# Kernel tuning notes

Measured on AMD Instinct MI355X. Metric: run time of the kernel, lower is better.

## Reference

```python
import jax, jax.numpy as jnp
import numpy as np

N, E, C, H = 50000, 800000, 64, 64
EPS = 1e-5


def _edge_conv(x, src, dst, Wa, ba, Wb, bb):
    # PyG EdgeConv: h_i = max_{j in N(i)} MLP([x_i, x_j - x_i]), aggr='max'
    xi = x[dst]                      # [E, C] target features
    xj = x[src]                      # [E, C] source features
    h = jnp.concatenate([xi, xj - xi], axis=-1)   # [E, 2C]
    h = jax.nn.relu(h @ Wa + ba)
    h = jax.nn.relu(h @ Wb + bb)     # [E, H]
    out = jax.ops.segment_max(h, dst, num_segments=x.shape[0])
    # nodes with no incoming edge: segment_max yields -inf -> fill with 0
    return jnp.where(jnp.isneginf(out), 0.0, out)


def _batchnorm(x, gamma, beta):
    # training-mode BatchNorm1d: biased batch stats over the node dim
    mean = jnp.mean(x, axis=0)
    var = jnp.var(x, axis=0)
    return gamma * (x - mean) * jax.lax.rsqrt(var + EPS) + beta


def setup_inputs() -> dict:
    key = jax.random.key(0)
    ks = jax.random.split(key, 12)
    x = jax.random.normal(ks[0], (N, C), dtype=jnp.float32)
    edge_index = jax.random.randint(ks[1], (2, E), 0, N, dtype=jnp.int64)
    batch = jnp.zeros((N,), dtype=jnp.int64)
    s1 = 1.0 / np.sqrt(2 * C)
    s2 = 1.0 / np.sqrt(H)
    return {
        "x": x,
        "edge_index": edge_index,
        "batch": batch,
        "W1a": jax.random.normal(ks[2], (2 * C, H), jnp.float32) * s1,
        "b1a": jnp.zeros((H,), jnp.float32),
        "W1b": jax.random.normal(ks[3], (H, H), jnp.float32) * s2,
        "b1b": jnp.zeros((H,), jnp.float32),
        "gamma1": jnp.ones((H,), jnp.float32),
        "beta1": jnp.zeros((H,), jnp.float32),
        "W2a": jax.random.normal(ks[4], (2 * H, H), jnp.float32) * s2,
        "b2a": jnp.zeros((H,), jnp.float32),
        "W2b": jax.random.normal(ks[5], (H, H), jnp.float32) * s2,
        "b2b": jnp.zeros((H,), jnp.float32),
        "gamma2": jnp.ones((H,), jnp.float32),
        "beta2": jnp.zeros((H,), jnp.float32),
    }


def reference(x, edge_index, batch, W1a, b1a, W1b, b1b, gamma1, beta1,
              W2a, b2a, W2b, b2b, gamma2, beta2):
    src, dst = edge_index[0], edge_index[1]
    h = _edge_conv(x, src, dst, W1a, b1a, W1b, b1b)
    h = _batchnorm(h, gamma1, beta1)
    h = _edge_conv(h, src, dst, W2a, b2a, W2b, b2b)
    h = _batchnorm(h, gamma2, beta2)
    return h
```

## Files before the change

### kernel.cpp

```cpp
#include <hip/hip_runtime.h>
#include <hip/hip_bf16.h>

typedef float f32x4 __attribute__((ext_vector_type(4)));
typedef short s16x8 __attribute__((ext_vector_type(8)));

#define EPS 1e-5f

__device__ __forceinline__ unsigned short f32_to_bf16_rne(float f) {
    unsigned u = __float_as_uint(f);
    unsigned r = u + 0x7FFFu + ((u >> 16) & 1u);
    return (unsigned short)(r >> 16);
}

__device__ __forceinline__ unsigned cvtpk(float a, float b) {
    unsigned d;
    asm("v_cvt_pk_bf16_f32 %0, %1, %2" : "=v"(d) : "v"(a), "v"(b));
    return d;
}

#define DPPF(v, c) __int_as_float(__builtin_amdgcn_update_dpp(0, __float_as_int(v), (c), 0xF, 0xF, true))
#define SWZ4(v) __int_as_float(__builtin_amdgcn_ds_swizzle(__float_as_int(v), 0x101F))

__global__ void pack_all(const float* __restrict__ W1a, const float* __restrict__ W1b,
                         const float* __restrict__ W2a, const float* __restrict__ W2b,
                         unsigned short* __restrict__ p, float* __restrict__ stats,
                         int* __restrict__ count, int N) {
    int idx = blockIdx.x * 256 + threadIdx.x;
    if (idx < 24576) {
        int m = idx >> 12;
        int t = idx & 4095;
        int j = t & 7;
        int lane = (t >> 3) & 63;
        int mt = (t >> 9) & 3;
        int kc = t >> 11;
        int k = kc * 32 + (lane >> 4) * 8 + j;
        int c = mt * 16 + (lane & 15);
        float v;
        switch (m) {
            case 0: v = W1a[k * 64 + c] - W1a[(k + 64) * 64 + c]; break;
            case 1: v = W1a[(k + 64) * 64 + c]; break;
            case 2: v = W1b[k * 64 + c]; break;
            case 3: v = W2a[k * 64 + c] - W2a[(k + 64) * 64 + c]; break;
            case 4: v = W2a[(k + 64) * 64 + c]; break;
            default: v = W2b[k * 64 + c]; break;
        }
        p[idx] = f32_to_bf16_rne(v);
    } else if (idx < 24832) {
        stats[idx - 24576] = 0.f;
    } else if (idx - 24832 < N) {
        count[idx - 24832] = 0;
    }
}

__global__ void cvt_hist(const float* __restrict__ in, unsigned short* __restrict__ out, int n4,
                         const int* __restrict__ edst, int* __restrict__ count, int E) {
    int i = blockIdx.x * 256 + threadIdx.x;
    if (i < n4) {
        f32x4 v = ((const f32x4*)in)[i];
        uint2 pr;
        pr.x = cvtpk(v[0], v[1]);
        pr.y = cvtpk(v[2], v[3]);
        *(uint2*)(out + i * 4) = pr;
    }
    if (i < E) atomicAdd(&count[edst[i]], 1);
}

__global__ void scan1(const int* __restrict__ count, int* __restrict__ offsets,
                      int* __restrict__ bsums, int N) {
    __shared__ int sdata[256];
    int t = threadIdx.x;
    int base = blockIdx.x * 1024 + t * 4;
    int4 v = {0, 0, 0, 0};
    if (base + 3 < N) {
        v = *(const int4*)(count + base);
    } else {
        if (base + 0 < N) v.x = count[base + 0];
        if (base + 1 < N) v.y = count[base + 1];
        if (base + 2 < N) v.z = count[base + 2];
    }
    int s = v.x + v.y + v.z + v.w;
    sdata[t] = s;
    __syncthreads();
    for (int off = 1; off < 256; off <<= 1) {
        int u = (t >= off) ? sdata[t - off] : 0;
        __syncthreads();
        sdata[t] += u;
        __syncthreads();
    }
    int excl = sdata[t] - s;
    if (t == 255) bsums[blockIdx.x] = sdata[255];
    int o0 = excl;
    int o1 = o0 + v.x;
    int o2 = o1 + v.y;
    int o3 = o2 + v.z;
    if (base + 0 < N) offsets[base + 0] = o0;
    if (base + 1 < N) offsets[base + 1] = o1;
    if (base + 2 < N) offsets[base + 2] = o2;
    if (base + 3 < N) offsets[base + 3] = o3;
}

__global__ void scan2(int* __restrict__ bsums, int* __restrict__ offsets, int N, int nb) {
    __shared__ int sdata[256];
    int t = threadIdx.x;
    int s = (t < nb) ? bsums[t] : 0;
    sdata[t] = s;
    __syncthreads();
    for (int off = 1; off < 256; off <<= 1) {
        int u = (t >= off) ? sdata[t - off] : 0;
        __syncthreads();
        sdata[t] += u;
        __syncthreads();
    }
    if (t < nb) bsums[t] = sdata[t] - s;
    if (t == 255) offsets[N] = sdata[255];
}

__global__ void scan3(int* __restrict__ offsets, int* __restrict__ cursor,
                      const int* __restrict__ bsums, int N) {
    int i = blockIdx.x * 256 + threadIdx.x;
    if (i < N) {
        int v = offsets[i] + bsums[i >> 10];
        offsets[i] = v;
        cursor[i] = v;
    }
}

__global__ void scatter_kernel(const int* __restrict__ esrc, const int* __restrict__ edst,
                               int* __restrict__ cursor, int* __restrict__ ssrc, int E) {
    int i = blockIdx.x * 256 + threadIdx.x;
    if (i < E) {
        int d = edst[i];
        int pos = atomicAdd(&cursor[d], 1);
        ssrc[pos] = esrc[i];
    }
}

#define LSTR 88
__global__ __launch_bounds__(256, 3) void edgeconv_sorted(
    const unsigned short* __restrict__ xb,
    const int* __restrict__ ssrc,
    const int* __restrict__ offsets,
    const unsigned short* __restrict__ pWxi,
    const unsigned short* __restrict__ pWxj,
    const unsigned short* __restrict__ pWb,
    const float* __restrict__ ba,
    const float* __restrict__ bb,
    float* __restrict__ out,
    float* __restrict__ statsOut,
    int N) {
    __shared__ __align__(16) unsigned short xh[4][16 * LSTR];
    __shared__ float sred[128];
    const int tid = threadIdx.x;
    const int w = tid >> 6;
    const int lane = tid & 63;
    const int g = lane >> 4;
    const int r = lane & 15;
    const int srow = lane >> 2;
    const int schk = lane & 3;

    if (tid < 128) sred[tid] = 0.f;
    __syncthreads();

    s16x8 axj[2][4], ab[2][4];
#pragma unroll
    for (int kc = 0; kc < 2; ++kc)
#pragma unroll
        for (int mt = 0; mt < 4; ++mt) {
            axj[kc][mt] = *(const s16x8*)(pWxj + ((kc * 4 + mt) * 64 + lane) * 8);
            ab[kc][mt] = *(const s16x8*)(pWb + ((kc * 4 + mt) * 64 + lane) * 8);
        }

    unsigned short* myb = xh[w];
    const int totalWaves = gridDim.x * 4;
    const f32x4 zf = {0.f, 0.f, 0.f, 0.f};

    const int ch = (r >> 2) * 16 + g * 4 + (r & 3);
    const float b2l = bb[ch];
    float bsum = 0.f, bss = 0.f;

    for (int node = blockIdx.x * 4 + w; node < N; node += totalWaves) {
        const int segB = offsets[node];
        const int segE = offsets[node + 1];

        f32x4 rm[4];
#pragma unroll
        for (int mt = 0; mt < 4; ++mt)
            rm[mt] = (f32x4){-INFINITY, -INFINITY, -INFINITY, -INFINITY};

        if (segB < segE) {
            int sv = ssrc[min(segB + srow, segE - 1)];
            s16x8 ra = *(const s16x8*)(xb + sv * 64 + schk * 8);
            s16x8 rb = *(const s16x8*)(xb + sv * 64 + 32 + schk * 8);

            s16x8 xi1 = *(const s16x8*)(xb + node * 64 + g * 8);
            s16x8 xi2 = *(const s16x8*)(xb + node * 64 + 32 + g * 8);
            f32x4 accxi[4];
#pragma unroll
            for (int mt = 0; mt < 4; ++mt)
                accxi[mt] = *(const f32x4*)(ba + mt * 16 + g * 4);
#pragma unroll
            for (int mt = 0; mt < 4; ++mt) {
                s16x8 f0 = *(const s16x8*)(pWxi + ((0 * 4 + mt) * 64 + lane) * 8);
                accxi[mt] = __builtin_amdgcn_mfma_f32_16x16x32_bf16(f0, xi1, accxi[mt], 0, 0, 0);
                s16x8 f1 = *(const s16x8*)(pWxi + ((1 * 4 + mt) * 64 + lane) * 8);
                accxi[mt] = __builtin_amdgcn_mfma_f32_16x16x32_bf16(f1, xi2, accxi[mt], 0, 0, 0);
            }

            for (int t0 = segB; t0 < segE; t0 += 16) {
                *(s16x8*)(myb + srow * LSTR + schk * 8) = ra;
                *(s16x8*)(myb + srow * LSTR + 32 + schk * 8) = rb;
                s16x8 xj1 = *(const s16x8*)(myb + r * LSTR + g * 8);
                s16x8 xj2 = *(const s16x8*)(myb + r * LSTR + 32 + g * 8);

                int t1 = t0 + 16;
                if (t1 < segE) {
                    int sv2 = ssrc[min(t1 + srow, segE - 1)];
                    ra = *(const s16x8*)(xb + sv2 * 64 + schk * 8);
                    rb = *(const s16x8*)(xb + sv2 * 64 + 32 + schk * 8);
                }

                f32x4 acc[4];
#pragma unroll
                for (int mt = 0; mt < 4; ++mt) {
                    acc[mt] = __builtin_amdgcn_mfma_f32_16x16x32_bf16(axj[0][mt], xj1, accxi[mt], 0, 0, 0);
                    acc[mt] = __builtin_amdgcn_mfma_f32_16x16x32_bf16(axj[1][mt], xj2, acc[mt], 0, 0, 0);
                }

#pragma unroll
                for (int mt = 0; mt < 4; ++mt) {
                    uint2 pr;
                    pr.x = cvtpk(fmaxf(acc[mt][0], 0.f), fmaxf(acc[mt][1], 0.f));
                    pr.y = cvtpk(fmaxf(acc[mt][2], 0.f), fmaxf(acc[mt][3], 0.f));
                    *(uint2*)(myb + r * LSTR + mt * 16 + g * 4) = pr;
                }
                s16x8 p0 = *(const s16x8*)(myb + r * LSTR + g * 8);
                s16x8 p1 = *(const s16x8*)(myb + r * LSTR + 32 + g * 8);

                f32x4 acc2[4];
#pragma unroll
                for (int mt = 0; mt < 4; ++mt) {
                    acc2[mt] = __builtin_amdgcn_mfma_f32_16x16x32_bf16(ab[0][mt], p0, zf, 0, 0, 0);
                    acc2[mt] = __builtin_amdgcn_mfma_f32_16x16x32_bf16(ab[1][mt], p1, acc2[mt], 0, 0, 0);
                }

#pragma unroll
                for (int mt = 0; mt < 4; ++mt)
#pragma unroll
                    for (int q = 0; q < 4; ++q)
                        rm[mt][q] = fmaxf(rm[mt][q], acc2[mt][q]);
            }
        }

        float k8[8];
#pragma unroll
        for (int j = 0; j < 8; ++j) {
            float lo = rm[j >> 2][j & 3];
            float hv = rm[(j >> 2) + 2][j & 3];
            float tlo = DPPF(lo, 0x128);
            float thi = DPPF(hv, 0x128);
            float own = (r & 8) ? hv : lo;
            float oth = (r & 8) ? thi : tlo;
            k8[j] = fmaxf(own, oth);
        }
        float k4[4];
#pragma unroll
        for (int j = 0; j < 4; ++j) {
            float ta = SWZ4(k8[j]);
            float tb = SWZ4(k8[j + 4]);
            float own = (r & 4) ? k8[j + 4] : k8[j];
            float oth = (r & 4) ? tb : ta;
            k4[j] = fmaxf(own, oth);
        }
        float k2[2];
#pragma unroll
        for (int j = 0; j < 2; ++j) {
            float ta = DPPF(k4[j], 0x4E);
            float tb = DPPF(k4[j + 2], 0x4E);
            float own = (r & 2) ? k4[j + 2] : k4[j];
            float oth = (r & 2) ? tb : ta;
            k2[j] = fmaxf(own, oth);
        }
        float ta = DPPF(k2[0], 0xB1);
        float tb = DPPF(k2[1], 0xB1);
        float vfin = fmaxf((r & 1) ? k2[1] : k2[0], (r & 1) ? tb : ta);

        float o = fmaxf(vfin + b2l, 0.f);
        out[node * 64 + ch] = o;
        bsum += o;
        bss += o * o;
    }

    atomicAdd(&sred[ch], bsum);
    atomicAdd(&sred[64 + ch], bss);
    __syncthreads();
    if (tid < 128) atomicAdd(&statsOut[tid], sred[tid]);
}

__global__ void bn_apply(const float* __restrict__ in, const float* __restrict__ stats,
                         const float* __restrict__ gamma, const float* __restrict__ beta,
                         unsigned short* __restrict__ outb, float* __restrict__ outf,
                         int n4, float invN) {
    int i = blockIdx.x * 256 + threadIdx.x;
    if (i >= n4) return;
    int c0 = (i * 4) & 63;
    f32x4 v = ((const f32x4*)in)[i];
    f32x4 o;
#pragma unroll
    for (int q = 0; q < 4; ++q) {
        int c = c0 + q;
        float mean = stats[c] * invN;
        float var = stats[64 + c] * invN - mean * mean;
        float sc = gamma[c] * rsqrtf(var + EPS);
        o[q] = (v[q] - mean) * sc + beta[c];
    }
    if (outb) {
        uint2 pr;
        pr.x = cvtpk(o[0], o[1]);
        pr.y = cvtpk(o[2], o[3]);
        *(uint2*)(outb + i * 4) = pr;
    } else {
        ((f32x4*)outf)[i] = o;
    }
}

extern "C" void kernel_launch(void* const* d_in, const int* in_sizes, int n_in,
                              void* d_out, int out_size, void* d_ws, size_t ws_size,
                              hipStream_t stream) {
    const float* x = (const float*)d_in[0];
    const int* ei = (const int*)d_in[1];
    const float* W1a = (const float*)d_in[3];
    const float* b1a = (const float*)d_in[4];
    const float* W1b = (const float*)d_in[5];
    const float* b1b = (const float*)d_in[6];
    const float* gamma1 = (const float*)d_in[7];
    const float* beta1 = (const float*)d_in[8];
    const float* W2a = (const float*)d_in[9];
    const float* b2a = (const float*)d_in[10];
    const float* W2b = (const float*)d_in[11];
    const float* b2b = (const float*)d_in[12];
    const float* gamma2 = (const float*)d_in[13];
    const float* beta2 = (const float*)d_in[14];

    const int N = in_sizes[0] / 64;
    const int E = in_sizes[1] / 2;
    const int NC = N * 64;

    char* ws = (char*)d_ws;
    size_t off = 0;
    auto alloc = [&](size_t bytes) {
        char* p = ws + off;
        off += (bytes + 255) & ~(size_t)255;
        return p;
    };
    float* acc = (float*)alloc((size_t)NC * 4);
    unsigned short* xb = (unsigned short*)alloc((size_t)NC * 2);
    unsigned short* pw = (unsigned short*)alloc(24576 * 2);
    float* stats = (float*)alloc(256 * 4);
    int* count = (int*)alloc((size_t)N * 4);
    int* offsets = (int*)alloc((size_t)(N + 1) * 4);
    int* cursor = (int*)alloc((size_t)(N + 1) * 4);
    int* ssrc = (int*)alloc((size_t)E * 4);
    int* bsums = (int*)alloc(1024 * 4);

    const int* esrc = ei;
    const int* edst = ei + E;

    int pgrid = (24832 + N + 255) / 256;
    pack_all<<<pgrid, 256, 0, stream>>>(W1a, W1b, W2a, W2b, pw, stats, count, N);

    int n4 = NC / 4;
    int big = max(n4, E);
    cvt_hist<<<(big + 255) / 256, 256, 0, stream>>>(x, xb, n4, edst, count, E);

    int nb = (N + 1023) / 1024;
    scan1<<<nb, 256, 0, stream>>>(count, offsets, bsums, N);
    scan2<<<1, 256, 0, stream>>>(bsums, offsets, N, nb);
    scan3<<<(N + 255) / 256, 256, 0, stream>>>(offsets, cursor, bsums, N);
    scatter_kernel<<<(E + 255) / 256, 256, 0, stream>>>(esrc, edst, cursor, ssrc, E);

    int cgrid = (n4 + 255) / 256;
    const int egrid = 2048;

    edgeconv_sorted<<<egrid, 256, 0, stream>>>(xb, ssrc, offsets, pw, pw + 4096, pw + 8192,
                                               b1a, b1b, acc, stats, N);
    bn_apply<<<cgrid, 256, 0, stream>>>(acc, stats, gamma1, beta1, xb, nullptr, n4, 1.0f / N);

    edgeconv_sorted<<<egrid, 256, 0, stream>>>(xb, ssrc, offsets, pw + 12288, pw + 16384,
                                               pw + 20480, b2a, b2b, (float*)d_out, stats + 128, N);
    bn_apply<<<cgrid, 256, 0, stream>>>((float*)d_out, stats + 128, gamma2, beta2, nullptr,
                                        (float*)d_out, n4, 1.0f / N);
}
```

Baseline: 267.6 us.

## Process two destination nodes per wave iteration to interleave independent MFMA chains

Each wave now handles a contiguous block of nodes, two at a time. The two nodes' gathers, MFMA chains, LDS staging and max-reductions are interleaved in one loop whose trip count is the larger of the two tile counts. The aim is to hide MFMA dependency latency and gather latency by giving the scheduler two independent streams of work. In exchange, the shorter segment does redundant work up to the longer one's tile count, register pressure roughly doubles, LDS per wave doubles, and the grid shrinks to 1792 blocks with a contiguous node partition.

```diff
diff --git a/kernel.cpp b/kernel.cpp
--- a/kernel.cpp
+++ b/kernel.cpp
@@ -147,8 +147,8 @@
     const float* __restrict__ bb,
     float* __restrict__ out,
     float* __restrict__ statsOut,
-    int N) {
-    __shared__ __align__(16) unsigned short xh[4][16 * LSTR];
+    int N, int npw) {
+    __shared__ __align__(16) unsigned short xh[4][2 * 16 * LSTR];
     __shared__ float sred[128];
     const int tid = threadIdx.x;
     const int w = tid >> 6;
@@ -170,124 +170,184 @@
             ab[kc][mt] = *(const s16x8*)(pWb + ((kc * 4 + mt) * 64 + lane) * 8);
         }
 
-    unsigned short* myb = xh[w];
-    const int totalWaves = gridDim.x * 4;
+    unsigned short* mybA = xh[w];
+    unsigned short* mybB = xh[w] + 16 * LSTR;
     const f32x4 zf = {0.f, 0.f, 0.f, 0.f};
 
     const int ch = (r >> 2) * 16 + g * 4 + (r & 3);
     const float b2l = bb[ch];
     float bsum = 0.f, bss = 0.f;
 
-    for (int node = blockIdx.x * 4 + w; node < N; node += totalWaves) {
-        const int segB = offsets[node];
-        const int segE = offsets[node + 1];
-
-        f32x4 rm[4];
+    const int wid = blockIdx.x * 4 + w;
+    const int nodeBase = wid * npw;
+    const int pairs = npw >> 1;
+
+    for (int p = 0; p < pairs; ++p) {
+        const int nA = nodeBase + 2 * p;
+        if (nA >= N) break;
+        const int nB = nA + 1;
+        const bool hasB = nB < N;
+
+        const int sBA = offsets[nA];
+        const int sEA = offsets[nA + 1];
+        const int sBB = hasB ? sEA : sBA;
+        const int sEB = hasB ? offsets[nB + 1] : sEA;
+        const bool vA = sEA > sBA;
+        const bool vB = hasB && (sEB > sBB);
+        const int ntA = max(1, (sEA - sBA + 15) >> 4);
+        const int ntB = max(1, (sEB - sBB + 15) >> 4);
+        const int nt = max(ntA, ntB);
+
+        int ivA = max(min(sBA + srow, sEA - 1), 0);
+        int ivB = max(min(sBB + srow, sEB - 1), 0);
+        int svA = ssrc[ivA];
+        int svB = ssrc[ivB];
+        s16x8 raA = *(const s16x8*)(xb + svA * 64 + schk * 8);
+        s16x8 rbA = *(const s16x8*)(xb + svA * 64 + 32 + schk * 8);
+        s16x8 raB = *(const s16x8*)(xb + svB * 64 + schk * 8);
+        s16x8 rbB = *(const s16x8*)(xb + svB * 64 + 32 + schk * 8);
+
+        const int rowB = min(nB, N - 1);
+        s16x8 xiA1 = *(const s16x8*)(xb + nA * 64 + g * 8);
+        s16x8 xiA2 = *(const s16x8*)(xb + nA * 64 + 32 + g * 8);
+        s16x8 xiB1 = *(const s16x8*)(xb + rowB * 64 + g * 8);
+        s16x8 xiB2 = *(const s16x8*)(xb + rowB * 64 + 32 + g * 8);
+        f32x4 accxiA[4], accxiB[4];
+#pragma unroll
+        for (int mt = 0; mt < 4; ++mt) {
+            f32x4 bias = *(const f32x4*)(ba + mt * 16 + g * 4);
+            s16x8 f0 = *(const s16x8*)(pWxi + ((0 * 4 + mt) * 64 + lane) * 8);
+            s16x8 f1 = *(const s16x8*)(pWxi + ((1 * 4 + mt) * 64 + lane) * 8);
+            f32x4 cA = __builtin_amdgcn_mfma_f32_16x16x32_bf16(f0, xiA1, bias, 0, 0, 0);
+            accxiA[mt] = __builtin_amdgcn_mfma_f32_16x16x32_bf16(f1, xiA2, cA, 0, 0, 0);
+            f32x4 cB = __builtin_amdgcn_mfma_f32_16x16x32_bf16(f0, xiB1, bias, 0, 0, 0);
+            accxiB[mt] = __builtin_amdgcn_mfma_f32_16x16x32_bf16(f1, xiB2, cB, 0, 0, 0);
+        }
+
+        f32x4 rmA[4], rmB[4];
+#pragma unroll
+        for (int mt = 0; mt < 4; ++mt) {
+            rmA[mt] = (f32x4){-INFINITY, -INFINITY, -INFINITY, -INFINITY};
+            rmB[mt] = (f32x4){-INFINITY, -INFINITY, -INFINITY, -INFINITY};
+        }
+
+        for (int it = 0; it < nt; ++it) {
+            *(s16x8*)(mybA + srow * LSTR + schk * 8) = raA;
+            *(s16x8*)(mybA + srow * LSTR + 32 + schk * 8) = rbA;
+            *(s16x8*)(mybB + srow * LSTR + schk * 8) = raB;
+            *(s16x8*)(mybB + srow * LSTR + 32 + schk * 8) = rbB;
+            s16x8 xjA1 = *(const s16x8*)(mybA + r * LSTR + g * 8);
+            s16x8 xjA2 = *(const s16x8*)(mybA + r * LSTR + 32 + g * 8);
+            s16x8 xjB1 = *(const s16x8*)(mybB + r * LSTR + g * 8);
+            s16x8 xjB2 = *(const s16x8*)(mybB + r * LSTR + 32 + g * 8);
+
+            if (it + 1 < nt) {
+                int tA2 = sBA + 16 * min(it + 1, ntA - 1);
+                int tB2 = sBB + 16 * min(it + 1, ntB - 1);
+                int iA2 = max(min(tA2 + srow, sEA - 1), 0);
+                int iB2 = max(min(tB2 + srow, sEB - 1), 0);
+                int sA2 = ssrc[iA2];
+                int sB2 = ssrc[iB2];
+                raA = *(const s16x8*)(xb + sA2 * 64 + schk * 8);
+                rbA = *(const s16x8*)(xb + sA2 * 64 + 32 + schk * 8);
+                raB = *(const s16x8*)(xb + sB2 * 64 + schk * 8);
+                rbB = *(const s16x8*)(xb + sB2 * 64 + 32 + schk * 8);
+            }
+
+            f32x4 accA[4], accB[4];
+#pragma unroll
+            for (int mt = 0; mt < 4; ++mt) {
+                accA[mt] = __builtin_amdgcn_mfma_f32_16x16x32_bf16(axj[0][mt], xjA1, accxiA[mt], 0, 0, 0);
+                accA[mt] = __builtin_amdgcn_mfma_f32_16x16x32_bf16(axj[1][mt], xjA2, accA[mt], 0, 0, 0);
+                accB[mt] = __builtin_amdgcn_mfma_f32_16x16x32_bf16(axj[0][mt], xjB1, accxiB[mt], 0, 0, 0);
+                accB[mt] = __builtin_amdgcn_mfma_f32_16x16x32_bf16(axj[1][mt], xjB2, accB[mt], 0, 0, 0);
+            }
+
+#pragma unroll
+            for (int mt = 0; mt < 4; ++mt) {
+                uint2 prA, prB;
+                prA.x = cvtpk(fmaxf(accA[mt][0], 0.f), fmaxf(accA[mt][1], 0.f));
+                prA.y = cvtpk(fmaxf(accA[mt][2], 0.f), fmaxf(accA[mt][3], 0.f));
+                *(uint2*)(mybA + r * LSTR + mt * 16 + g * 4) = prA;
+                prB.x = cvtpk(fmaxf(accB[mt][0], 0.f), fmaxf(accB[mt][1], 0.f));
+                prB.y = cvtpk(fmaxf(accB[mt][2], 0.f), fmaxf(accB[mt][3], 0.f));
+                *(uint2*)(mybB + r * LSTR + mt * 16 + g * 4) = prB;
+            }
+            s16x8 pA0 = *(const s16x8*)(mybA + r * LSTR + g * 8);
+            s16x8 pA1 = *(const s16x8*)(mybA + r * LSTR + 32 + g * 8);
+            s16x8 pB0 = *(const s16x8*)(mybB + r * LSTR + g * 8);
+            s16x8 pB1 = *(const s16x8*)(mybB + r * LSTR + 32 + g * 8);
+
+            f32x4 acc2A[4], acc2B[4];
+#pragma unroll
+            for (int mt = 0; mt < 4; ++mt) {
+                acc2A[mt] = __builtin_amdgcn_mfma_f32_16x16x32_bf16(ab[0][mt], pA0, zf, 0, 0, 0);
+                acc2A[mt] = __builtin_amdgcn_mfma_f32_16x16x32_bf16(ab[1][mt], pA1, acc2A[mt], 0, 0, 0);
+                acc2B[mt] = __builtin_amdgcn_mfma_f32_16x16x32_bf16(ab[0][mt], pB0, zf, 0, 0, 0);
+                acc2B[mt] = __builtin_amdgcn_mfma_f32_16x16x32_bf16(ab[1][mt], pB1, acc2B[mt], 0, 0, 0);
+            }
+
+#pragma unroll
+            for (int mt = 0; mt < 4; ++mt)
+#pragma unroll
+                for (int q = 0; q < 4; ++q) {
+                    rmA[mt][q] = fmaxf(rmA[mt][q], acc2A[mt][q]);
+                    rmB[mt][q] = fmaxf(rmB[mt][q], acc2B[mt][q]);
+                }
+        }
+
 #pragma unroll
         for (int mt = 0; mt < 4; ++mt)
-            rm[mt] = (f32x4){-INFINITY, -INFINITY, -INFINITY, -INFINITY};
-
-        if (segB < segE) {
-            int sv = ssrc[min(segB + srow, segE - 1)];
-            s16x8 ra = *(const s16x8*)(xb + sv * 64 + schk * 8);
-            s16x8 rb = *(const s16x8*)(xb + sv * 64 + 32 + schk * 8);
-
-            s16x8 xi1 = *(const s16x8*)(xb + node * 64 + g * 8);
-            s16x8 xi2 = *(const s16x8*)(xb + node * 64 + 32 + g * 8);
-            f32x4 accxi[4];
-#pragma unroll
-            for (int mt = 0; mt < 4; ++mt)
-                accxi[mt] = *(const f32x4*)(ba + mt * 16 + g * 4);
-#pragma unroll
-            for (int mt = 0; mt < 4; ++mt) {
-                s16x8 f0 = *(const s16x8*)(pWxi + ((0 * 4 + mt) * 64 + lane) * 8);
-                accxi[mt] = __builtin_amdgcn_mfma_f32_16x16x32_bf16(f0, xi1, accxi[mt], 0, 0, 0);
-                s16x8 f1 = *(const s16x8*)(pWxi + ((1 * 4 + mt) * 64 + lane) * 8);
-                accxi[mt] = __builtin_amdgcn_mfma_f32_16x16x32_bf16(f1, xi2, accxi[mt], 0, 0, 0);
-            }
-
-            for (int t0 = segB; t0 < segE; t0 += 16) {
-                *(s16x8*)(myb + srow * LSTR + schk * 8) = ra;
-                *(s16x8*)(myb + srow * LSTR + 32 + schk * 8) = rb;
-                s16x8 xj1 = *(const s16x8*)(myb + r * LSTR + g * 8);
-                s16x8 xj2 = *(const s16x8*)(myb + r * LSTR + 32 + g * 8);
-
-                int t1 = t0 + 16;
-                if (t1 < segE) {
-                    int sv2 = ssrc[min(t1 + srow, segE - 1)];
-                    ra = *(const s16x8*)(xb + sv2 * 64 + schk * 8);
-                    rb = *(const s16x8*)(xb + sv2 * 64 + 32 + schk * 8);
-                }
-
-                f32x4 acc[4];
-#pragma unroll
-                for (int mt = 0; mt < 4; ++mt) {
-                    acc[mt] = __builtin_amdgcn_mfma_f32_16x16x32_bf16(axj[0][mt], xj1, accxi[mt], 0, 0, 0);
-                    acc[mt] = __builtin_amdgcn_mfma_f32_16x16x32_bf16(axj[1][mt], xj2, acc[mt], 0, 0, 0);
-                }
-
-#pragma unroll
-                for (int mt = 0; mt < 4; ++mt) {
-                    uint2 pr;
-                    pr.x = cvtpk(fmaxf(acc[mt][0], 0.f), fmaxf(acc[mt][1], 0.f));
-                    pr.y = cvtpk(fmaxf(acc[mt][2], 0.f), fmaxf(acc[mt][3], 0.f));
-                    *(uint2*)(myb + r * LSTR + mt * 16 + g * 4) = pr;
-                }
-                s16x8 p0 = *(const s16x8*)(myb + r * LSTR + g * 8);
-                s16x8 p1 = *(const s16x8*)(myb + r * LSTR + 32 + g * 8);
-
-                f32x4 acc2[4];
-#pragma unroll
-                for (int mt = 0; mt < 4; ++mt) {
-                    acc2[mt] = __builtin_amdgcn_mfma_f32_16x16x32_bf16(ab[0][mt], p0, zf, 0, 0, 0);
-                    acc2[mt] = __builtin_amdgcn_mfma_f32_16x16x32_bf16(ab[1][mt], p1, acc2[mt], 0, 0, 0);
-                }
-
-#pragma unroll
-                for (int mt = 0; mt < 4; ++mt)
-#pragma unroll
-                    for (int q = 0; q < 4; ++q)
-                        rm[mt][q] = fmaxf(rm[mt][q], acc2[mt][q]);
-            }
-        }
-
-        float k8[8];
-#pragma unroll
-        for (int j = 0; j < 8; ++j) {
-            float lo = rm[j >> 2][j & 3];
-            float hv = rm[(j >> 2) + 2][j & 3];
-            float tlo = DPPF(lo, 0x128);
-            float thi = DPPF(hv, 0x128);
-            float own = (r & 8) ? hv : lo;
-            float oth = (r & 8) ? thi : tlo;
-            k8[j] = fmaxf(own, oth);
-        }
-        float k4[4];
-#pragma unroll
-        for (int j = 0; j < 4; ++j) {
-            float ta = SWZ4(k8[j]);
-            float tb = SWZ4(k8[j + 4]);
-            float own = (r & 4) ? k8[j + 4] : k8[j];
-            float oth = (r & 4) ? tb : ta;
-            k4[j] = fmaxf(own, oth);
-        }
-        float k2[2];
-#pragma unroll
-        for (int j = 0; j < 2; ++j) {
-            float ta = DPPF(k4[j], 0x4E);
-            float tb = DPPF(k4[j + 2], 0x4E);
-            float own = (r & 2) ? k4[j + 2] : k4[j];
-            float oth = (r & 2) ? tb : ta;
-            k2[j] = fmaxf(own, oth);
-        }
-        float ta = DPPF(k2[0], 0xB1);
-        float tb = DPPF(k2[1], 0xB1);
-        float vfin = fmaxf((r & 1) ? k2[1] : k2[0], (r & 1) ? tb : ta);
-
-        float o = fmaxf(vfin + b2l, 0.f);
-        out[node * 64 + ch] = o;
-        bsum += o;
-        bss += o * o;
+#pragma unroll
+            for (int q = 0; q < 4; ++q) {
+                rmA[mt][q] = vA ? rmA[mt][q] : -INFINITY;
+                rmB[mt][q] = vB ? rmB[mt][q] : -INFINITY;
+            }
+
+#pragma unroll
+        for (int nsel = 0; nsel < 2; ++nsel) {
+            const f32x4* rm = nsel ? rmB : rmA;
+            float k8[8];
+#pragma unroll
+            for (int j = 0; j < 8; ++j) {
+                float lo = rm[j >> 2][j & 3];
+                float hv = rm[(j >> 2) + 2][j & 3];
+                float tlo = DPPF(lo, 0x128);
+                float thi = DPPF(hv, 0x128);
+                float own = (r & 8) ? hv : lo;
+                float oth = (r & 8) ? thi : tlo;
+                k8[j] = fmaxf(own, oth);
+            }
+            float k4[4];
+#pragma unroll
+            for (int j = 0; j < 4; ++j) {
+                float ta = SWZ4(k8[j]);
+                float tb = SWZ4(k8[j + 4]);
+                float own = (r & 4) ? k8[j + 4] : k8[j];
+                float oth = (r & 4) ? tb : ta;
+                k4[j] = fmaxf(own, oth);
+            }
+            float k2[2];
+#pragma unroll
+            for (int j = 0; j < 2; ++j) {
+                float ta = DPPF(k4[j], 0x4E);
+                float tb = DPPF(k4[j + 2], 0x4E);
+                float own = (r & 2) ? k4[j + 2] : k4[j];
+                float oth = (r & 2) ? tb : ta;
+                k2[j] = fmaxf(own, oth);
+            }
+            float ta = DPPF(k2[0], 0xB1);
+            float tb = DPPF(k2[1], 0xB1);
+            float vfin = fmaxf((r & 1) ? k2[1] : k2[0], (r & 1) ? tb : ta);
+
+            float o = fmaxf(vfin + b2l, 0.f);
+            int node = nsel ? nB : nA;
+            if (!nsel || hasB) {
+                out[node * 64 + ch] = o;
+                bsum += o;
+                bss += o * o;
+            }
+        }
     }
 
     atomicAdd(&sred[ch], bsum);
@@ -379,14 +439,18 @@
     scatter_kernel<<<(E + 255) / 256, 256, 0, stream>>>(esrc, edst, cursor, ssrc, E);
 
     int cgrid = (n4 + 255) / 256;
-    const int egrid = 2048;
+    const int egrid = 1792;
+    const int tw = egrid * 4;
+    int npw = (N + tw - 1) / tw;
+    npw = ((npw + 1) / 2) * 2;
 
     edgeconv_sorted<<<egrid, 256, 0, stream>>>(xb, ssrc, offsets, pw, pw + 4096, pw + 8192,
-                                               b1a, b1b, acc, stats, N);
+                                               b1a, b1b, acc, stats, N, npw);
     bn_apply<<<cgrid, 256, 0, stream>>>(acc, stats, gamma1, beta1, xb, nullptr, n4, 1.0f / N);
 
     edgeconv_sorted<<<egrid, 256, 0, stream>>>(xb, ssrc, offsets, pw + 12288, pw + 16384,
-                                               pw + 20480, b2a, b2b, (float*)d_out, stats + 128, N);
+                                               pw + 20480, b2a, b2b, (float*)d_out, stats + 128,
+                                               N, npw);
     bn_apply<<<cgrid, 256, 0, stream>>>((float*)d_out, stats + 128, gamma2, beta2, nullptr,
                                         (float*)d_out, n4, 1.0f / N);
 }
```

Result: slower. 405.3 us (+51.4%).

## Prefetch next node's segment and features; keep Wxi and bias in registers

Applied to the files above, without the earlier changes.

The edgeconv loop now loads the next node's offsets, first source-row features and own features while the current node is being processed, hiding gather latency across loop iterations. The Wxi weight fragments and first-layer bias are hoisted into registers once instead of being reloaded per node. The extra live registers force launch bounds to drop from 3 to 2 waves-per-SIMD minimum, which lowers occupancy in exchange for software pipelining.

```diff
diff --git a/kernel.cpp b/kernel.cpp
--- a/kernel.cpp
+++ b/kernel.cpp
@@ -136,7 +136,7 @@
 }
 
 #define LSTR 88
-__global__ __launch_bounds__(256, 3) void edgeconv_sorted(
+__global__ __launch_bounds__(256, 2) void edgeconv_sorted(
     const unsigned short* __restrict__ xb,
     const int* __restrict__ ssrc,
     const int* __restrict__ offsets,
@@ -161,14 +161,18 @@
     if (tid < 128) sred[tid] = 0.f;
     __syncthreads();
 
-    s16x8 axj[2][4], ab[2][4];
+    s16x8 awxi[2][4], axj[2][4], ab[2][4];
 #pragma unroll
     for (int kc = 0; kc < 2; ++kc)
 #pragma unroll
         for (int mt = 0; mt < 4; ++mt) {
+            awxi[kc][mt] = *(const s16x8*)(pWxi + ((kc * 4 + mt) * 64 + lane) * 8);
             axj[kc][mt] = *(const s16x8*)(pWxj + ((kc * 4 + mt) * 64 + lane) * 8);
             ab[kc][mt] = *(const s16x8*)(pWb + ((kc * 4 + mt) * 64 + lane) * 8);
         }
+    f32x4 bias1r[4];
+#pragma unroll
+    for (int mt = 0; mt < 4; ++mt) bias1r[mt] = *(const f32x4*)(ba + mt * 16 + g * 4);
 
     unsigned short* myb = xh[w];
     const int totalWaves = gridDim.x * 4;
@@ -178,9 +182,34 @@
     const float b2l = bb[ch];
     float bsum = 0.f, bss = 0.f;
 
-    for (int node = blockIdx.x * 4 + w; node < N; node += totalWaves) {
-        const int segB = offsets[node];
-        const int segE = offsets[node + 1];
+    const int node0 = blockIdx.x * 4 + w;
+    int segB = 0, segE = 0;
+    s16x8 ra = {}, rb = {}, xi1 = {}, xi2 = {};
+    if (node0 < N) {
+        segB = offsets[node0];
+        segE = offsets[node0 + 1];
+        int iv = max(min(segB + srow, segE - 1), 0);
+        int sv = ssrc[iv];
+        ra = *(const s16x8*)(xb + sv * 64 + schk * 8);
+        rb = *(const s16x8*)(xb + sv * 64 + 32 + schk * 8);
+        xi1 = *(const s16x8*)(xb + node0 * 64 + g * 8);
+        xi2 = *(const s16x8*)(xb + node0 * 64 + 32 + g * 8);
+    }
+
+    for (int node = node0; node < N; node += totalWaves) {
+        const int nodeN = node + totalWaves;
+        int segBn = 0, segEn = 0;
+        s16x8 ran = {}, rbn = {}, xin1 = {}, xin2 = {};
+        if (nodeN < N) {
+            segBn = offsets[nodeN];
+            segEn = offsets[nodeN + 1];
+            int ivn = max(min(segBn + srow, segEn - 1), 0);
+            int svn = ssrc[ivn];
+            ran = *(const s16x8*)(xb + svn * 64 + schk * 8);
+            rbn = *(const s16x8*)(xb + svn * 64 + 32 + schk * 8);
+            xin1 = *(const s16x8*)(xb + nodeN * 64 + g * 8);
+            xin2 = *(const s16x8*)(xb + nodeN * 64 + 32 + g * 8);
+        }
 
         f32x4 rm[4];
 #pragma unroll
@@ -188,22 +217,11 @@
             rm[mt] = (f32x4){-INFINITY, -INFINITY, -INFINITY, -INFINITY};
 
         if (segB < segE) {
-            int sv = ssrc[min(segB + srow, segE - 1)];
-            s16x8 ra = *(const s16x8*)(xb + sv * 64 + schk * 8);
-            s16x8 rb = *(const s16x8*)(xb + sv * 64 + 32 + schk * 8);
-
-            s16x8 xi1 = *(const s16x8*)(xb + node * 64 + g * 8);
-            s16x8 xi2 = *(const s16x8*)(xb + node * 64 + 32 + g * 8);
             f32x4 accxi[4];
 #pragma unroll
-            for (int mt = 0; mt < 4; ++mt)
-                accxi[mt] = *(const f32x4*)(ba + mt * 16 + g * 4);
-#pragma unroll
             for (int mt = 0; mt < 4; ++mt) {
-                s16x8 f0 = *(const s16x8*)(pWxi + ((0 * 4 + mt) * 64 + lane) * 8);
-                accxi[mt] = __builtin_amdgcn_mfma_f32_16x16x32_bf16(f0, xi1, accxi[mt], 0, 0, 0);
-                s16x8 f1 = *(const s16x8*)(pWxi + ((1 * 4 + mt) * 64 + lane) * 8);
-                accxi[mt] = __builtin_amdgcn_mfma_f32_16x16x32_bf16(f1, xi2, accxi[mt], 0, 0, 0);
+                f32x4 c = __builtin_amdgcn_mfma_f32_16x16x32_bf16(awxi[0][mt], xi1, bias1r[mt], 0, 0, 0);
+                accxi[mt] = __builtin_amdgcn_mfma_f32_16x16x32_bf16(awxi[1][mt], xi2, c, 0, 0, 0);
             }
 
             for (int t0 = segB; t0 < segE; t0 += 16) {
@@ -288,6 +306,13 @@
         out[node * 64 + ch] = o;
         bsum += o;
         bss += o * o;
+
+        segB = segBn;
+        segE = segEn;
+        ra = ran;
+        rb = rbn;
+        xi1 = xin1;
+        xi2 = xin2;
     }
 
     atomicAdd(&sred[ch], bsum);
```

New measurement: 275.4 us. 1.03x slower.

## Fold first BatchNorm into second EdgeConv weights and bias

Applied to the files above, without the earlier changes.

Drops the first bn_apply pass. The first EdgeConv now writes its raw ReLU output straight to bf16, and a small single-block kernel scales the second layer's W2a rows by the BN scale and folds the BN shift into an adjusted bias. This holds because BN is affine per channel and feeds linearly into the first matmul, and the shift cancels in the x_j - x_i half. It removes one full read-fp32/write-bf16 pass over the node features and one launch. The cost is a serial one-block repack kernel and bf16 rounding applied before normalization rather than after, which could change accuracy somewhat.

```diff
diff --git a/kernel.cpp b/kernel.cpp
--- a/kernel.cpp
+++ b/kernel.cpp
@@ -21,12 +21,11 @@
 #define DPPF(v, c) __int_as_float(__builtin_amdgcn_update_dpp(0, __float_as_int(v), (c), 0xF, 0xF, true))
 #define SWZ4(v) __int_as_float(__builtin_amdgcn_ds_swizzle(__float_as_int(v), 0x101F))
 
-__global__ void pack_all(const float* __restrict__ W1a, const float* __restrict__ W1b,
-                         const float* __restrict__ W2a, const float* __restrict__ W2b,
-                         unsigned short* __restrict__ p, float* __restrict__ stats,
-                         int* __restrict__ count, int N) {
+__global__ void pack_zero(const float* __restrict__ W1a, const float* __restrict__ W1b,
+                          const float* __restrict__ W2b, unsigned short* __restrict__ p,
+                          float* __restrict__ stats, int* __restrict__ count, int N) {
     int idx = blockIdx.x * 256 + threadIdx.x;
-    if (idx < 24576) {
+    if (idx < 16384) {
         int m = idx >> 12;
         int t = idx & 4095;
         int j = t & 7;
@@ -36,19 +35,18 @@
         int k = kc * 32 + (lane >> 4) * 8 + j;
         int c = mt * 16 + (lane & 15);
         float v;
+        int dst;
         switch (m) {
-            case 0: v = W1a[k * 64 + c] - W1a[(k + 64) * 64 + c]; break;
-            case 1: v = W1a[(k + 64) * 64 + c]; break;
-            case 2: v = W1b[k * 64 + c]; break;
-            case 3: v = W2a[k * 64 + c] - W2a[(k + 64) * 64 + c]; break;
-            case 4: v = W2a[(k + 64) * 64 + c]; break;
-            default: v = W2b[k * 64 + c]; break;
-        }
-        p[idx] = f32_to_bf16_rne(v);
-    } else if (idx < 24832) {
-        stats[idx - 24576] = 0.f;
-    } else if (idx - 24832 < N) {
-        count[idx - 24832] = 0;
+            case 0: v = W1a[k * 64 + c] - W1a[(k + 64) * 64 + c]; dst = t; break;
+            case 1: v = W1a[(k + 64) * 64 + c]; dst = 4096 + t; break;
+            case 2: v = W1b[k * 64 + c]; dst = 8192 + t; break;
+            default: v = W2b[k * 64 + c]; dst = 20480 + t; break;
+        }
+        p[dst] = f32_to_bf16_rne(v);
+    } else if (idx < 16640) {
+        stats[idx - 16384] = 0.f;
+    } else if (idx - 16640 < N) {
+        count[idx - 16640] = 0;
     }
 }
 
@@ -135,6 +133,51 @@
     }
 }
 
+__global__ void repack2(const float* __restrict__ stats, const float* __restrict__ gamma1,
+                        const float* __restrict__ beta1, const float* __restrict__ W2a,
+                        const float* __restrict__ b2a, unsigned short* __restrict__ pw2,
+                        float* __restrict__ b2adj, float invN) {
+    __shared__ float sc[64], sh[64];
+    __shared__ float part[4][64];
+    int tid = threadIdx.x;
+    if (tid < 64) {
+        float mean = stats[tid] * invN;
+        float var = stats[64 + tid] * invN - mean * mean;
+        float s = gamma1[tid] * rsqrtf(var + EPS);
+        sc[tid] = s;
+        sh[tid] = beta1[tid] - mean * s;
+    }
+    __syncthreads();
+    {
+        int c = tid & 63, sl = tid >> 6;
+        float a = 0.f;
+#pragma unroll
+        for (int kk = 0; kk < 16; ++kk) {
+            int k = sl * 16 + kk;
+            a += sh[k] * W2a[k * 64 + c];
+        }
+        part[sl][c] = a;
+    }
+    __syncthreads();
+    if (tid < 64)
+        b2adj[tid] = b2a[tid] + part[0][tid] + part[1][tid] + part[2][tid] + part[3][tid];
+
+    for (int e = tid; e < 8192; e += 256) {
+        int m = e >> 12;
+        int t = e & 4095;
+        int j = t & 7;
+        int lane = (t >> 3) & 63;
+        int mt = (t >> 9) & 3;
+        int kc = t >> 11;
+        int k = kc * 32 + (lane >> 4) * 8 + j;
+        int c = mt * 16 + (lane & 15);
+        float wtop = W2a[k * 64 + c];
+        float wbot = W2a[(k + 64) * 64 + c];
+        float v = (m == 0) ? sc[k] * (wtop - wbot) : sc[k] * wbot;
+        pw2[e] = f32_to_bf16_rne(v);
+    }
+}
+
 #define LSTR 88
 __global__ __launch_bounds__(256, 3) void edgeconv_sorted(
     const unsigned short* __restrict__ xb,
@@ -145,7 +188,8 @@
     const unsigned short* __restrict__ pWb,
     const float* __restrict__ ba,
     const float* __restrict__ bb,
-    float* __restrict__ out,
+    float* __restrict__ outf,
+    unsigned short* __restrict__ outb,
     float* __restrict__ statsOut,
     int N) {
     __shared__ __align__(16) unsigned short xh[4][16 * LSTR];
@@ -285,7 +329,10 @@
         float vfin = fmaxf((r & 1) ? k2[1] : k2[0], (r & 1) ? tb : ta);
 
         float o = fmaxf(vfin + b2l, 0.f);
-        out[node * 64 + ch] = o;
+        if (outb)
+            outb[node * 64 + ch] = f32_to_bf16_rne(o);
+        else
+            outf[node * 64 + ch] = o;
         bsum += o;
         bss += o * o;
     }
@@ -298,8 +345,7 @@
 
 __global__ void bn_apply(const float* __restrict__ in, const float* __restrict__ stats,
                          const float* __restrict__ gamma, const float* __restrict__ beta,
-                         unsigned short* __restrict__ outb, float* __restrict__ outf,
-                         int n4, float invN) {
+                         float* __restrict__ outf, int n4, float invN) {
     int i = blockIdx.x * 256 + threadIdx.x;
     if (i >= n4) return;
     int c0 = (i * 4) & 63;
@@ -313,14 +359,7 @@
         float sc = gamma[c] * rsqrtf(var + EPS);
         o[q] = (v[q] - mean) * sc + beta[c];
     }
-    if (outb) {
-        uint2 pr;
-        pr.x = cvtpk(o[0], o[1]);
-        pr.y = cvtpk(o[2], o[3]);
-        *(uint2*)(outb + i * 4) = pr;
-    } else {
-        ((f32x4*)outf)[i] = o;
-    }
+    ((f32x4*)outf)[i] = o;
 }
 
 extern "C" void kernel_launch(void* const* d_in, const int* in_sizes, int n_in,
@@ -352,10 +391,11 @@
         off += (bytes + 255) & ~(size_t)255;
         return p;
     };
-    float* acc = (float*)alloc((size_t)NC * 4);
-    unsigned short* xb = (unsigned short*)alloc((size_t)NC * 2);
+    unsigned short* xb1 = (unsigned short*)alloc((size_t)NC * 2);
+    unsigned short* xb2 = (unsigned short*)alloc((size_t)NC * 2);
     unsigned short* pw = (unsigned short*)alloc(24576 * 2);
     float* stats = (float*)alloc(256 * 4);
+    float* b2adj = (float*)alloc(64 * 4);
     int* count = (int*)alloc((size_t)N * 4);
     int* offsets = (int*)alloc((size_t)(N + 1) * 4);
     int* cursor = (int*)alloc((size_t)(N + 1) * 4);
@@ -365,12 +405,12 @@
     const int* esrc = ei;
     const int* edst = ei + E;
 
-    int pgrid = (24832 + N + 255) / 256;
-    pack_all<<<pgrid, 256, 0, stream>>>(W1a, W1b, W2a, W2b, pw, stats, count, N);
+    int pgrid = (16640 + N + 255) / 256;
+    pack_zero<<<pgrid, 256, 0, stream>>>(W1a, W1b, W2b, pw, stats, count, N);
 
     int n4 = NC / 4;
     int big = max(n4, E);
-    cvt_hist<<<(big + 255) / 256, 256, 0, stream>>>(x, xb, n4, edst, count, E);
+    cvt_hist<<<(big + 255) / 256, 256, 0, stream>>>(x, xb1, n4, edst, count, E);
 
     int nb = (N + 1023) / 1024;
     scan1<<<nb, 256, 0, stream>>>(count, offsets, bsums, N);
@@ -378,15 +418,18 @@
     scan3<<<(N + 255) / 256, 256, 0, stream>>>(offsets, cursor, bsums, N);
     scatter_kernel<<<(E + 255) / 256, 256, 0, stream>>>(esrc, edst, cursor, ssrc, E);
 
+    const int egrid = 2048;
+
+    edgeconv_sorted<<<egrid, 256, 0, stream>>>(xb1, ssrc, offsets, pw, pw + 4096, pw + 8192,
+                                               b1a, b1b, nullptr, xb2, stats, N);
+
+    repack2<<<1, 256, 0, stream>>>(stats, gamma1, beta1, W2a, b2a, pw + 12288, b2adj, 1.0f / N);
+
+    edgeconv_sorted<<<egrid, 256, 0, stream>>>(xb2, ssrc, offsets, pw + 12288, pw + 16384,
+                                               pw + 20480, b2adj, b2b, (float*)d_out, nullptr,
+                                               stats + 128, N);
+
     int cgrid = (n4 + 255) / 256;
-    const int egrid = 2048;
-
-    edgeconv_sorted<<<egrid, 256, 0, stream>>>(xb, ssrc, offsets, pw, pw + 4096, pw + 8192,
-                                               b1a, b1b, acc, stats, N);
-    bn_apply<<<cgrid, 256, 0, stream>>>(acc, stats, gamma1, beta1, xb, nullptr, n4, 1.0f / N);
-
-    edgeconv_sorted<<<egrid, 256, 0, stream>>>(xb, ssrc, offsets, pw + 12288, pw + 16384,
-                                               pw + 20480, b2a, b2b, (float*)d_out, stats + 128, N);
-    bn_apply<<<cgrid, 256, 0, stream>>>((float*)d_out, stats + 128, gamma2, beta2, nullptr,
+    bn_apply<<<cgrid, 256, 0, stream>>>((float*)d_out, stats + 128, gamma2, beta2,
                                         (float*)d_out, n4, 1.0f / N);
 }
```

New measurement: 268.1 us. About the same (+0.2%).
